# Kernel optimization log

Measured on AMD Instinct MI355X. Metric: run time of the kernel, lower is better.

## Reference

```python
import jax, jax.numpy as jnp
import numpy as np

B, S, D = 128, 512, 768          # batch, seq_len, token_dim
NH, HD = 8, 96                    # num_heads, head_dim = sentence_dim/num_heads
HID = 4 * HD                      # hidden_dim = 384


def setup_inputs() -> dict:
    key = jax.random.key(0)
    ks = jax.random.split(key, 9)
    token_embeddings = jax.random.normal(ks[0], (B, S, D), dtype=jnp.float32)
    # variable-length attention mask (1 for real tokens, 0 for padding)
    lengths = jax.random.randint(ks[1], (B,), S // 2, S + 1)
    attention_mask = (jnp.arange(S)[None, :] < lengths[:, None]).astype(jnp.float32)
    s = 0.02
    P  = jax.random.normal(ks[2], (NH, HD, D),   dtype=jnp.float32) * s
    bP = jnp.zeros((NH, HD), dtype=jnp.float32)
    W1 = jax.random.normal(ks[3], (NH, HID, HD), dtype=jnp.float32) * s
    b1 = jnp.zeros((NH, HID), dtype=jnp.float32)
    W2 = jax.random.normal(ks[4], (NH, HD, HID), dtype=jnp.float32) * s
    b2 = jnp.zeros((NH, HD), dtype=jnp.float32)
    return {"token_embeddings": token_embeddings, "attention_mask": attention_mask,
            "P": P, "bP": bP, "W1": W1, "b1": b1, "W2": W2, "b2": b2}


def reference(token_embeddings, attention_mask, P, bP, W1, b1, W2, b2):
    # per-head projection: H_i = P_i(H)           -> (nh, B, S, HD)
    Hi = jnp.einsum('bsd,ihd->ibsh', token_embeddings, P) + bP[:, None, None, :]
    # scores: W2(relu(W1(H_i)))                   -> (nh, B, S, HD)
    A = jnp.einsum('ibsf,ihf->ibsh',
                   jax.nn.relu(jnp.einsum('ibsh,ifh->ibsf', Hi, W1) + b1[:, None, None, :]),
                   W2) + b2[:, None, None, :]
    # masked softmax over sequence dim (log(mask) adds -inf on padding)
    log_mask = jnp.log(attention_mask)[None, :, :, None]  # (1, B, S, 1)
    A = jax.nn.softmax(A + log_mask, axis=2)
    # weighted sum over tokens                    -> (nh, B, HD)
    v = jnp.sum(Hi * A, axis=2)
    # concat heads: (B, nh*HD) = (B, 768)
    pooled = jnp.transpose(v, (1, 0, 2)).reshape(token_embeddings.shape[0], NH * HD)
    return pooled
```

## Files before the change

kernel.cpp:

```cpp
#include <hip/hip_runtime.h>
#include <stdint.h>


typedef short bf16x8 __attribute__((ext_vector_type(8)));
typedef float f32x4 __attribute__((ext_vector_type(4)));

struct alignas(8) us4 { unsigned short x, y, z, w; };

__device__ __forceinline__ unsigned short f32_to_bf16(float f) {
  union { float f; uint32_t u; } v; v.f = f;
  uint32_t u = v.u;
  uint32_t r = (u + 0x7fffu + ((u >> 16) & 1u)) >> 16;
  return (unsigned short)r;
}

__device__ __forceinline__ float bf16_to_f32(unsigned short h) {
  union { uint32_t u; float f; } v; v.u = ((uint32_t)h) << 16;
  return v.f;
}

__device__ __forceinline__ uint32_t pack_bf16_trunc(float lo, float hi) {
  union { float f; uint32_t u; } a, b; a.f = lo; b.f = hi;
  return __builtin_amdgcn_perm(b.u, a.u, 0x07060302u);
}

__device__ __forceinline__ void g2l16(const unsigned short* g, unsigned short* l) {
  __builtin_amdgcn_global_load_lds((__attribute__((address_space(1))) void*)g,
                                   (__attribute__((address_space(3))) void*)l,
                                   16, 0, 0);
}


#define N_X   50331648
#define N_P   589824
#define N_W1  294912
#define N_W2  294912
#define N_HI  50331648


__global__ __launch_bounds__(256) void cast_f32_bf16(
    const float* __restrict__ src, unsigned short* __restrict__ dst, int n4) {
  int idx = blockIdx.x * 256 + threadIdx.x;
  if (idx >= n4) return;
  float4 v = ((const float4*)src)[idx];
  us4 o;
  o.x = f32_to_bf16(v.x);
  o.y = f32_to_bf16(v.y);
  o.z = f32_to_bf16(v.z);
  o.w = f32_to_bf16(v.w);
  ((us4*)dst)[idx] = o;
}


__global__ __launch_bounds__(256) void repack_w1(
    const float* __restrict__ W1, unsigned short* __restrict__ W1bf) {
  const int quarter = blockIdx.x;
  const int hd = quarter >> 2, ph = quarter & 3;
  for (int t = threadIdx.x; t < 1152; t += 256) {
    const int kb = t / 384;
    const int rem = t - kb * 384;
    const int f = rem >> 2, slot = rem & 3;
    const int pos = slot ^ ((f >> 1) & 3);
    const float* src =
        W1 + ((size_t)(hd * 384 + ph * 96 + f)) * 96 + kb * 32 + pos * 8;
    float4 a = *(const float4*)src;
    float4 b = *(const float4*)(src + 4);
    us4 o1 = {f32_to_bf16(a.x), f32_to_bf16(a.y), f32_to_bf16(a.z), f32_to_bf16(a.w)};
    us4 o2 = {f32_to_bf16(b.x), f32_to_bf16(b.y), f32_to_bf16(b.z), f32_to_bf16(b.w)};
    us4* dst = (us4*)(W1bf + (size_t)quarter * 9216 + t * 8);
    dst[0] = o1;
    dst[1] = o2;
  }
}

__global__ __launch_bounds__(256) void repack_w2(
    const float* __restrict__ W2, unsigned short* __restrict__ W2bf) {
  const int quarter = blockIdx.x;
  const int hd = quarter >> 2, ph = quarter & 3;
  for (int t = threadIdx.x; t < 1152; t += 256) {
    const int kb = t / 384;
    const int rem = t - kb * 384;
    const int h = rem >> 2, slot = rem & 3;
    const int pos = slot ^ ((h >> 1) & 3);
    const float* src =
        W2 + ((size_t)(hd * 96 + h)) * 384 + ph * 96 + kb * 32 + pos * 8;
    float4 a = *(const float4*)src;
    float4 b = *(const float4*)(src + 4);
    us4 o1 = {f32_to_bf16(a.x), f32_to_bf16(a.y), f32_to_bf16(a.z), f32_to_bf16(a.w)};
    us4 o2 = {f32_to_bf16(b.x), f32_to_bf16(b.y), f32_to_bf16(b.z), f32_to_bf16(b.w)};
    us4* dst = (us4*)(W2bf + (size_t)quarter * 9216 + t * 8);
    dst[0] = o1;
    dst[1] = o2;
  }
}


__global__ __launch_bounds__(256) void gemm_hi(
    const unsigned short* __restrict__ Xbf,
    const unsigned short* __restrict__ Pbf,
    const float* __restrict__ bP,
    unsigned short* __restrict__ Hi) {
  __shared__ __align__(16) unsigned short As[128 * 32];
  __shared__ __align__(16) unsigned short Bs[128 * 32];

  const int tid = threadIdx.x;
  const int w = tid >> 6;
  const int lane = tid & 63;
  const int r = lane & 15;
  const int q = lane >> 4;

  const int hwid = blockIdx.x;
  const int wkid = (hwid & 7) * 384 + (hwid >> 3);
  const int bn = wkid % 6;
  const int bm = wkid / 6;

  const int wr = w >> 1, wc = w & 1;
  const int psw = q ^ ((r >> 1) & 3);

  f32x4 acc[4][4];
#pragma unroll
  for (int a = 0; a < 4; ++a)
#pragma unroll
    for (int c = 0; c < 4; ++c) acc[a][c] = (f32x4){0.f, 0.f, 0.f, 0.f};

  const int ldr = lane >> 2;
  const int ldc = ((lane & 3) ^ ((lane >> 3) & 3)) * 8;
  const unsigned short* Abase = Xbf + (size_t)(bm * 128) * 768 + ldc;
  const unsigned short* Bbase = Pbf + (size_t)(bn * 128) * 768 + ldc;

  for (int k0 = 0; k0 < 768; k0 += 32) {
    __syncthreads();
    g2l16(Abase + (size_t)(w * 16 + ldr) * 768 + k0, &As[w * 512]);
    g2l16(Abase + (size_t)(64 + w * 16 + ldr) * 768 + k0, &As[(4 + w) * 512]);
    g2l16(Bbase + (size_t)(w * 16 + ldr) * 768 + k0, &Bs[w * 512]);
    g2l16(Bbase + (size_t)(64 + w * 16 + ldr) * 768 + k0, &Bs[(4 + w) * 512]);
    __syncthreads();

    bf16x8 af[4], bfr[4];
#pragma unroll
    for (int t = 0; t < 4; ++t)
      af[t] = *(const bf16x8*)&As[(wr * 64 + t * 16 + r) * 32 + psw * 8];
#pragma unroll
    for (int t = 0; t < 4; ++t)
      bfr[t] = *(const bf16x8*)&Bs[(wc * 64 + t * 16 + r) * 32 + psw * 8];
#pragma unroll
    for (int mt = 0; mt < 4; ++mt)
#pragma unroll
      for (int nt = 0; nt < 4; ++nt)
        acc[mt][nt] = __builtin_amdgcn_mfma_f32_16x16x32_bf16(
            af[mt], bfr[nt], acc[mt][nt], 0, 0, 0);
  }

  const int bb = bm >> 2;
  const int sb = (bm & 3) * 128 + wr * 64;
#pragma unroll
  for (int nt = 0; nt < 4; ++nt) {
    const int n0 = bn * 128 + wc * 64 + nt * 16;
    const int hd = n0 / 96;
    const int hloc = n0 - hd * 96;
    const int kb = hloc >> 5;
    const int col = (hloc & 31) + r;
    const float bias = bP[n0 + r];
    unsigned short* obase =
        Hi + (size_t)(hd * 128 + bb) * 49152 + kb * 16384 + col;
#pragma unroll
    for (int mt = 0; mt < 4; ++mt) {
#pragma unroll
      for (int rg = 0; rg < 4; ++rg) {
        const int s = sb + mt * 16 + q * 4 + rg;
        obase[(size_t)s * 32] = f32_to_bf16(acc[mt][nt][rg] + bias);
      }
    }
  }
}


__global__ __launch_bounds__(256, 2) void mlp_pool(
    const unsigned short* __restrict__ Hi,
    const unsigned short* __restrict__ W1bf,
    const unsigned short* __restrict__ W2bf,
    const float* __restrict__ b1,
    const float* __restrict__ b2,
    const float* __restrict__ mask,
    float* __restrict__ out) {
  __shared__ __align__(16) unsigned short Ys[3 * 128 * 32];
  __shared__ __align__(16) unsigned short Ws[3 * 96 * 32];
  __shared__ __align__(16) unsigned short Fs[128 * 104];
  __shared__ __align__(16) float b1s[384];
  __shared__ __align__(16) float b2s[96];
  __shared__ float bias_s[512];
  __shared__ float redA[4][96];
  __shared__ float redB[4][96];

  const int x = blockIdx.x;
  const int b = x & 127;
  const int hd = x >> 7;

  const int tid = threadIdx.x;
  const int w = tid >> 6;
  const int lane = tid & 63;
  const int r = lane & 15;
  const int q = lane >> 4;
  const int psw = q ^ ((r >> 1) & 3);
  const int ysx = (tid ^ ((tid >> 3) & 3)) * 8;

  if (tid < 96) b2s[tid] = b2[hd * 96 + tid];
  for (int i = tid; i < 384; i += 256) b1s[i] = b1[hd * 384 + i];
  for (int s = tid; s < 512; s += 256)
    bias_s[s] = mask[b * 512 + s] > 0.5f ? 0.f : -1e30f;

  float m_run[6], l_run[6], v_run[6];
#pragma unroll
  for (int nt = 0; nt < 6; ++nt) { m_run[nt] = -3e30f; l_run[nt] = 0.f; v_run[nt] = 0.f; }

  const unsigned short* ysrc = Hi + (size_t)(hd * 128 + b) * 49152;

  for (int c = 0; c < 4; ++c) {
    __syncthreads();

    {
      const unsigned short* yc = ysrc + c * 4096 + ysx;
      g2l16(yc, &Ys[w * 512]);
      g2l16(yc + 2048, &Ys[(4 + w) * 512]);
      g2l16(yc + 16384, &Ys[(8 + w) * 512]);
      g2l16(yc + 18432, &Ys[(12 + w) * 512]);
      g2l16(yc + 32768, &Ys[(16 + w) * 512]);
      g2l16(yc + 34816, &Ys[(20 + w) * 512]);
    }

    f32x4 acc3[2][6];
#pragma unroll
    for (int sp = 0; sp < 2; ++sp)
#pragma unroll
      for (int nt = 0; nt < 6; ++nt) acc3[sp][nt] = (f32x4){0.f, 0.f, 0.f, 0.f};

    for (int ph = 0; ph < 4; ++ph) {
      if (ph) __syncthreads();

      const unsigned short* w1src = W1bf + (size_t)(hd * 4 + ph) * 9216;
#pragma unroll
      for (int it = 0; it < 4; ++it)
        g2l16(w1src + (size_t)((it * 4 + w) * 64 + lane) * 8, &Ws[(it * 4 + w) * 512]);
      if (w < 2)
        g2l16(w1src + (size_t)((16 + w) * 64 + lane) * 8, &Ws[(16 + w) * 512]);
      __syncthreads();

      f32x4 acc2[6][2];
#pragma unroll
      for (int ft = 0; ft < 6; ++ft)
#pragma unroll
        for (int sp = 0; sp < 2; ++sp) acc2[ft][sp] = (f32x4){0.f, 0.f, 0.f, 0.f};
#pragma unroll
      for (int kb = 0; kb < 3; ++kb) {
        bf16x8 bfrg[2];
#pragma unroll
        for (int sp = 0; sp < 2; ++sp)
          bfrg[sp] = *(const bf16x8*)&Ys[kb * 4096 + ((w * 2 + sp) * 16 + r) * 32 + psw * 8];
#pragma unroll
        for (int ft = 0; ft < 6; ++ft) {
          bf16x8 afrg = *(const bf16x8*)&Ws[kb * 3072 + (ft * 16 + r) * 32 + psw * 8];
#pragma unroll
          for (int sp = 0; sp < 2; ++sp)
            acc2[ft][sp] = __builtin_amdgcn_mfma_f32_16x16x32_bf16(
                afrg, bfrg[sp], acc2[ft][sp], 0, 0, 0);
        }
      }
#pragma unroll
      for (int ft = 0; ft < 6; ++ft) {
        float4 bv = *(const float4*)&b1s[ph * 96 + ft * 16 + q * 4];
#pragma unroll
        for (int sp = 0; sp < 2; ++sp) {
          const int s = (w * 2 + sp) * 16 + r;
          float v0 = fmaxf(acc2[ft][sp][0] + bv.x, 0.f);
          float v1 = fmaxf(acc2[ft][sp][1] + bv.y, 0.f);
          float v2 = fmaxf(acc2[ft][sp][2] + bv.z, 0.f);
          float v3 = fmaxf(acc2[ft][sp][3] + bv.w, 0.f);
          uint2 pk;
          pk.x = pack_bf16_trunc(v0, v1);
          pk.y = pack_bf16_trunc(v2, v3);
          *(uint2*)((uint32_t*)&Fs[0] + s * 52 + ft * 8 + q * 2) = pk;
        }
      }
      __syncthreads();

      const unsigned short* w2src = W2bf + (size_t)(hd * 4 + ph) * 9216;
#pragma unroll
      for (int it = 0; it < 4; ++it)
        g2l16(w2src + (size_t)((it * 4 + w) * 64 + lane) * 8, &Ws[(it * 4 + w) * 512]);
      if (w < 2)
        g2l16(w2src + (size_t)((16 + w) * 64 + lane) * 8, &Ws[(16 + w) * 512]);
      __syncthreads();

#pragma unroll
      for (int kb = 0; kb < 3; ++kb) {
        bf16x8 afrg[2];
#pragma unroll
        for (int sp = 0; sp < 2; ++sp)
          afrg[sp] = *(const bf16x8*)&Fs[((w * 2 + sp) * 16 + r) * 104 + kb * 32 + q * 8];
#pragma unroll
        for (int nt = 0; nt < 6; ++nt) {
          bf16x8 bfrg = *(const bf16x8*)&Ws[kb * 3072 + (nt * 16 + r) * 32 + psw * 8];
#pragma unroll
          for (int sp = 0; sp < 2; ++sp)
            acc3[sp][nt] = __builtin_amdgcn_mfma_f32_16x16x32_bf16(
                afrg[sp], bfrg, acc3[sp][nt], 0, 0, 0);
        }
      }
    }

#pragma unroll
    for (int nt = 0; nt < 6; ++nt) {
      const float b2v = b2s[nt * 16 + r];
      float lm = -3e30f;
#pragma unroll
      for (int sp = 0; sp < 2; ++sp) {
#pragma unroll
        for (int rg = 0; rg < 4; ++rg) {
          const int sl = (w * 2 + sp) * 16 + q * 4 + rg;
          float lg = acc3[sp][nt][rg] + b2v + bias_s[c * 128 + sl];
          lm = fmaxf(lm, lg);
        }
      }
      lm = fmaxf(lm, __shfl_xor(lm, 16));
      lm = fmaxf(lm, __shfl_xor(lm, 32));
      if (q == 0) redA[w][nt * 16 + r] = lm;
    }
    __syncthreads();
#pragma unroll
    for (int nt = 0; nt < 6; ++nt) {
      const int h = nt * 16 + r;
      const int kbh = nt >> 1;
      const int gh = (nt * 2 + (r >> 3)) & 3;
      const int hlo = r & 7;
      const float cm = fmaxf(fmaxf(redA[0][h], redA[1][h]),
                             fmaxf(redA[2][h], redA[3][h]));
      const float mnew = fmaxf(m_run[nt], cm);
      const float sc = __expf(m_run[nt] - mnew);
      m_run[nt] = mnew;
      float lacc = l_run[nt] * sc;
      float vacc = v_run[nt] * sc;
      const float b2v = b2s[h];
#pragma unroll
      for (int sp = 0; sp < 2; ++sp) {
#pragma unroll
        for (int rg = 0; rg < 4; ++rg) {
          const int sl = (w * 2 + sp) * 16 + q * 4 + rg;
          float lg = acc3[sp][nt][rg] + b2v + bias_s[c * 128 + sl];
          float e = __expf(lg - mnew);
          lacc += e;
          const int pos = gh ^ ((sl >> 1) & 3);
          vacc += e * bf16_to_f32(Ys[kbh * 4096 + sl * 32 + pos * 8 + hlo]);
        }
      }
      l_run[nt] = lacc;
      v_run[nt] = vacc;
    }
  }

  __syncthreads();
#pragma unroll
  for (int nt = 0; nt < 6; ++nt) {
    float ls = l_run[nt], vs = v_run[nt];
    ls += __shfl_xor(ls, 16);
    vs += __shfl_xor(vs, 16);
    ls += __shfl_xor(ls, 32);
    vs += __shfl_xor(vs, 32);
    if (q == 0) {
      redA[w][nt * 16 + r] = ls;
      redB[w][nt * 16 + r] = vs;
    }
  }
  __syncthreads();
  if (tid < 96) {
    float ls = redA[0][tid] + redA[1][tid] + redA[2][tid] + redA[3][tid];
    float vs = redB[0][tid] + redB[1][tid] + redB[2][tid] + redB[3][tid];
    out[(size_t)b * 768 + hd * 96 + tid] = vs / ls;
  }
}


extern "C" void kernel_launch(void* const* d_in, const int* in_sizes, int n_in,
                              void* d_out, int out_size, void* d_ws, size_t ws_size,
                              hipStream_t stream) {
  const float* X    = (const float*)d_in[0];
  const float* mask = (const float*)d_in[1];
  const float* P    = (const float*)d_in[2];
  const float* bP   = (const float*)d_in[3];
  const float* W1   = (const float*)d_in[4];
  const float* b1   = (const float*)d_in[5];
  const float* W2   = (const float*)d_in[6];
  const float* b2   = (const float*)d_in[7];
  float* out = (float*)d_out;
  (void)in_sizes; (void)n_in; (void)out_size; (void)ws_size;

  unsigned short* Xbf  = (unsigned short*)d_ws;
  unsigned short* Pbf  = Xbf + N_X;
  unsigned short* W1bf = Pbf + N_P;
  unsigned short* W2bf = W1bf + N_W1;
  unsigned short* Hi   = W2bf + N_W2;

  cast_f32_bf16<<<N_X / 4 / 256, 256, 0, stream>>>(X, Xbf, N_X / 4);
  cast_f32_bf16<<<N_P / 4 / 256, 256, 0, stream>>>(P, Pbf, N_P / 4);
  repack_w1<<<32, 256, 0, stream>>>(W1, W1bf);
  repack_w2<<<32, 256, 0, stream>>>(W2, W2bf);

  gemm_hi<<<3072, 256, 0, stream>>>(Xbf, Pbf, bP, Hi);
  mlp_pool<<<8 * 128, 256, 0, stream>>>(Hi, W1bf, W2bf, b1, b2, mask, out);
}
```

Measured before the change: 519.7 us.

## Double-buffer W1/W2 staging and read Hi fragments directly from global

Splits the single weight buffer into separate W1 and W2 LDS buffers. Each load is issued one phase ahead, so weight staging overlaps MFMA work and fewer barriers are needed per phase. The Hi tile is no longer staged in LDS: MFMA B-fragments are loaded straight from global memory each phase, and the pooling step also reads Hi from global. This removes LDS staging and barriers, but repeats global/L2 reads of Hi across the four phases and the pooling loop, and the per-element strided gathers there may be poorly coalesced.

```diff
diff --git a/kernel.cpp b/kernel.cpp
--- a/kernel.cpp
+++ b/kernel.cpp
@@ -28,6 +28,15 @@
   __builtin_amdgcn_global_load_lds((__attribute__((address_space(1))) void*)g,
                                    (__attribute__((address_space(3))) void*)l,
                                    16, 0, 0);
+}
+
+__device__ __forceinline__ void stageW(const unsigned short* __restrict__ src,
+                                       unsigned short* dst, int w, int lane) {
+#pragma unroll
+  for (int it = 0; it < 4; ++it)
+    g2l16(src + (size_t)((it * 4 + w) * 64 + lane) * 8, &dst[(it * 4 + w) * 512]);
+  if (w < 2)
+    g2l16(src + (size_t)((16 + w) * 64 + lane) * 8, &dst[(16 + w) * 512]);
 }
 
 
@@ -183,8 +192,8 @@
     const float* __restrict__ b2,
     const float* __restrict__ mask,
     float* __restrict__ out) {
-  __shared__ __align__(16) unsigned short Ys[3 * 128 * 32];
-  __shared__ __align__(16) unsigned short Ws[3 * 96 * 32];
+  __shared__ __align__(16) unsigned short Ws1[3 * 96 * 32];
+  __shared__ __align__(16) unsigned short Ws2[3 * 96 * 32];
   __shared__ __align__(16) unsigned short Fs[128 * 104];
   __shared__ __align__(16) float b1s[384];
   __shared__ __align__(16) float b2s[96];
@@ -202,7 +211,6 @@
   const int r = lane & 15;
   const int q = lane >> 4;
   const int psw = q ^ ((r >> 1) & 3);
-  const int ysx = (tid ^ ((tid >> 3) & 3)) * 8;
 
   if (tid < 96) b2s[tid] = b2[hd * 96 + tid];
   for (int i = tid; i < 384; i += 256) b1s[i] = b1[hd * 384 + i];
@@ -214,19 +222,14 @@
   for (int nt = 0; nt < 6; ++nt) { m_run[nt] = -3e30f; l_run[nt] = 0.f; v_run[nt] = 0.f; }
 
   const unsigned short* ysrc = Hi + (size_t)(hd * 128 + b) * 49152;
+  const unsigned short* w1h = W1bf + (size_t)(hd * 4) * 9216;
+  const unsigned short* w2h = W2bf + (size_t)(hd * 4) * 9216;
+
+  stageW(w1h, Ws1, w, lane);
+  __syncthreads();
 
   for (int c = 0; c < 4; ++c) {
-    __syncthreads();
-
-    {
-      const unsigned short* yc = ysrc + c * 4096 + ysx;
-      g2l16(yc, &Ys[w * 512]);
-      g2l16(yc + 2048, &Ys[(4 + w) * 512]);
-      g2l16(yc + 16384, &Ys[(8 + w) * 512]);
-      g2l16(yc + 18432, &Ys[(12 + w) * 512]);
-      g2l16(yc + 32768, &Ys[(16 + w) * 512]);
-      g2l16(yc + 34816, &Ys[(20 + w) * 512]);
-    }
+    const unsigned short* yc = ysrc + c * 4096;
 
     f32x4 acc3[2][6];
 #pragma unroll
@@ -235,15 +238,15 @@
       for (int nt = 0; nt < 6; ++nt) acc3[sp][nt] = (f32x4){0.f, 0.f, 0.f, 0.f};
 
     for (int ph = 0; ph < 4; ++ph) {
-      if (ph) __syncthreads();
-
-      const unsigned short* w1src = W1bf + (size_t)(hd * 4 + ph) * 9216;
-#pragma unroll
-      for (int it = 0; it < 4; ++it)
-        g2l16(w1src + (size_t)((it * 4 + w) * 64 + lane) * 8, &Ws[(it * 4 + w) * 512]);
-      if (w < 2)
-        g2l16(w1src + (size_t)((16 + w) * 64 + lane) * 8, &Ws[(16 + w) * 512]);
-      __syncthreads();
+      bf16x8 bfrg[2][3];
+#pragma unroll
+      for (int sp = 0; sp < 2; ++sp)
+#pragma unroll
+        for (int kb = 0; kb < 3; ++kb)
+          bfrg[sp][kb] = *(const bf16x8*)(yc + kb * 16384 +
+                                          ((w * 2 + sp) * 16 + r) * 32 + q * 8);
+
+      stageW(w2h + ph * 9216, Ws2, w, lane);
 
       f32x4 acc2[6][2];
 #pragma unroll
@@ -252,17 +255,13 @@
         for (int sp = 0; sp < 2; ++sp) acc2[ft][sp] = (f32x4){0.f, 0.f, 0.f, 0.f};
 #pragma unroll
       for (int kb = 0; kb < 3; ++kb) {
-        bf16x8 bfrg[2];
-#pragma unroll
-        for (int sp = 0; sp < 2; ++sp)
-          bfrg[sp] = *(const bf16x8*)&Ys[kb * 4096 + ((w * 2 + sp) * 16 + r) * 32 + psw * 8];
 #pragma unroll
         for (int ft = 0; ft < 6; ++ft) {
-          bf16x8 afrg = *(const bf16x8*)&Ws[kb * 3072 + (ft * 16 + r) * 32 + psw * 8];
+          bf16x8 afrg = *(const bf16x8*)&Ws1[kb * 3072 + (ft * 16 + r) * 32 + psw * 8];
 #pragma unroll
           for (int sp = 0; sp < 2; ++sp)
             acc2[ft][sp] = __builtin_amdgcn_mfma_f32_16x16x32_bf16(
-                afrg, bfrg[sp], acc2[ft][sp], 0, 0, 0);
+                afrg, bfrg[sp][kb], acc2[ft][sp], 0, 0, 0);
         }
       }
 #pragma unroll
@@ -283,13 +282,8 @@
       }
       __syncthreads();
 
-      const unsigned short* w2src = W2bf + (size_t)(hd * 4 + ph) * 9216;
-#pragma unroll
-      for (int it = 0; it < 4; ++it)
-        g2l16(w2src + (size_t)((it * 4 + w) * 64 + lane) * 8, &Ws[(it * 4 + w) * 512]);
-      if (w < 2)
-        g2l16(w2src + (size_t)((16 + w) * 64 + lane) * 8, &Ws[(16 + w) * 512]);
-      __syncthreads();
+      if (!(c == 3 && ph == 3))
+        stageW(w1h + ((ph + 1) & 3) * 9216, Ws1, w, lane);
 
 #pragma unroll
       for (int kb = 0; kb < 3; ++kb) {
@@ -299,13 +293,14 @@
           afrg[sp] = *(const bf16x8*)&Fs[((w * 2 + sp) * 16 + r) * 104 + kb * 32 + q * 8];
 #pragma unroll
         for (int nt = 0; nt < 6; ++nt) {
-          bf16x8 bfrg = *(const bf16x8*)&Ws[kb * 3072 + (nt * 16 + r) * 32 + psw * 8];
+          bf16x8 bfrg2 = *(const bf16x8*)&Ws2[kb * 3072 + (nt * 16 + r) * 32 + psw * 8];
 #pragma unroll
           for (int sp = 0; sp < 2; ++sp)
             acc3[sp][nt] = __builtin_amdgcn_mfma_f32_16x16x32_bf16(
-                afrg[sp], bfrg, acc3[sp][nt], 0, 0, 0);
+                afrg[sp], bfrg2, acc3[sp][nt], 0, 0, 0);
         }
       }
+      __syncthreads();
     }
 
 #pragma unroll
@@ -329,9 +324,7 @@
 #pragma unroll
     for (int nt = 0; nt < 6; ++nt) {
       const int h = nt * 16 + r;
-      const int kbh = nt >> 1;
-      const int gh = (nt * 2 + (r >> 3)) & 3;
-      const int hlo = r & 7;
+      const unsigned short* yb = yc + (nt >> 1) * 16384 + (nt & 1) * 16 + r;
       const float cm = fmaxf(fmaxf(redA[0][h], redA[1][h]),
                              fmaxf(redA[2][h], redA[3][h]));
       const float mnew = fmaxf(m_run[nt], cm);
@@ -348,8 +341,7 @@
           float lg = acc3[sp][nt][rg] + b2v + bias_s[c * 128 + sl];
           float e = __expf(lg - mnew);
           lacc += e;
-          const int pos = gh ^ ((sl >> 1) & 3);
-          vacc += e * bf16_to_f32(Ys[kbh * 4096 + sl * 32 + pos * 8 + hlo]);
+          vacc += e * bf16_to_f32(yb[(size_t)sl * 32]);
         }
       }
       l_run[nt] = lacc;
```

New measurement: 542.3 us. 4.3% more time.
